# Kernel tuning notes

Hardware: AMD Instinct MI355X
Metric: run time of the kernel (lower is better)

## Reference

```python
import jax, jax.numpy as jnp
import numpy as np

MUL0, MUL1 = 32, 16          # multiplicities of 0e and 1o in irreps_node
RBF, HID = 16, 64
O1 = MUL0 * MUL0             # path 0e x 0e -> 0e
O2 = O1 + MUL0 * MUL1        # path 0e x 1o -> 1o
O3 = O2 + MUL1 * MUL1        # path 1o x 0e -> 1o
WNUMEL = O3 + MUL1 * MUL0    # path 1o x 1o -> 0e  => 2304 total
C_PATH = 1.0 / np.sqrt(MUL0 + MUL1).astype(np.float32)  # per-output fan-in norm
C_110 = 1.0 / np.sqrt(3.0)   # CG factor for 1o x 1o -> 0e (component norm)


def setup_inputs() -> dict:
    key = jax.random.key(0)
    ks = jax.random.split(key, 16)
    N, E = 50000, 200000
    x = jax.random.normal(ks[0], (N, MUL0 + 3 * MUL1), jnp.float32)
    edge_src = jax.random.randint(ks[1], (E,), 0, N)
    edge_dst = jax.random.randint(ks[2], (E,), 0, N)
    edge_sh = jax.random.normal(ks[3], (E, 4), jnp.float32)
    edge_rbf = jax.random.uniform(ks[4], (E, RBF), jnp.float32)
    # RadialMLP params (fan-in scaled init)
    w1 = jax.random.normal(ks[5], (RBF, HID), jnp.float32) / np.sqrt(RBF)
    b1 = jnp.zeros((HID,), jnp.float32)
    w2 = jax.random.normal(ks[6], (HID, HID), jnp.float32) / np.sqrt(HID)
    b2 = jnp.zeros((HID,), jnp.float32)
    w3 = jax.random.normal(ks[7], (HID, WNUMEL), jnp.float32) / np.sqrt(HID)
    b3 = jnp.zeros((WNUMEL,), jnp.float32)
    # o3.Linear weights (per-irrep mixing, fan-in normalization folded in)
    ws_self = jax.random.normal(ks[8], (MUL0, MUL0), jnp.float32) / np.sqrt(MUL0)
    wv_self = jax.random.normal(ks[9], (MUL1, MUL1), jnp.float32) / np.sqrt(MUL1)
    ws_out = jax.random.normal(ks[10], (MUL0, MUL0), jnp.float32) / np.sqrt(MUL0)
    wv_out = jax.random.normal(ks[11], (MUL1, MUL1), jnp.float32) / np.sqrt(MUL1)
    return {"x": x, "edge_src": edge_src, "edge_dst": edge_dst,
            "edge_sh": edge_sh, "edge_rbf": edge_rbf,
            "w1": w1, "b1": b1, "w2": w2, "b2": b2, "w3": w3, "b3": b3,
            "ws_self": ws_self, "wv_self": wv_self,
            "ws_out": ws_out, "wv_out": wv_out}


def _irrep_linear(x, ws, wv):
    # per-irrep mixing of '32x0e + 16x1o' features; x: [N, 80]
    n = x.shape[0]
    s = x[:, :MUL0] @ ws                                     # [N, 32]
    v = jnp.einsum('nid,io->nod', x[:, MUL0:].reshape(n, MUL1, 3), wv)
    return jnp.concatenate([s, v.reshape(n, 3 * MUL1)], axis=-1)


def reference(x, edge_src, edge_dst, edge_sh, edge_rbf,
              w1, b1, w2, b2, w3, b3, ws_self, wv_self, ws_out, wv_out):
    N = x.shape[0]
    E = edge_rbf.shape[0]
    # radial MLP -> per-edge TP weights [E, 2304]
    h = jax.nn.silu(edge_rbf @ w1 + b1)
    h = jax.nn.silu(h @ w2 + b2)
    W = h @ w3 + b3
    W1 = W[:, :O1].reshape(E, MUL0, MUL0)      # 0e x 0e -> 0e
    W2 = W[:, O1:O2].reshape(E, MUL0, MUL1)    # 0e x 1o -> 1o
    W3 = W[:, O2:O3].reshape(E, MUL1, MUL1)    # 1o x 0e -> 1o
    W4 = W[:, O3:].reshape(E, MUL1, MUL0)      # 1o x 1o -> 0e
    # gather source node features per edge
    xs = x[edge_src, :MUL0]                                   # [E, 32]
    xv = x[edge_src, MUL0:].reshape(E, MUL1, 3)               # [E, 16, 3]
    sh_s = edge_sh[:, 0]                                      # [E]
    sh_v = edge_sh[:, 1:4]                                    # [E, 3]
    # CG tensor product paths
    out_s = jnp.einsum('ei,eio->eo', xs * sh_s[:, None], W1)
    out_s = out_s + C_110 * jnp.einsum('eid,ed,eio->eo', xv, sh_v, W4)
    out_v = jnp.einsum('ei,ed,eio->eod', xs, sh_v, W2)
    out_v = out_v + jnp.einsum('eid,eio->eod', xv * sh_s[:, None, None], W3)
    m = C_PATH * jnp.concatenate([out_s, out_v.reshape(E, 3 * MUL1)], axis=-1)
    # scatter-add + degree normalize
    agg = jax.ops.segment_sum(m, edge_dst, num_segments=N)
    deg = jax.ops.segment_sum(jnp.ones((E,), x.dtype), edge_dst, num_segments=N)
    agg = agg / jnp.maximum(deg, 1.0)[:, None]
    return _irrep_linear(x, ws_self, wv_self) + _irrep_linear(agg, ws_out, wv_out)
```

## Files before the change

kernel.cpp:

```cpp
#include <hip/hip_runtime.h>
#include <math.h>

#define MUL0    32
#define MUL1    16
#define RBFD    16
#define HIDD    64
#define WNUMEL  2304
#define FDIM    80
#define CPATH   0.14433756729740643f
#define C110    0.57735026918962576f

#define TE       160
#define NTHREADS 320
#define NITER    48

#define W3N_ELEMS (NITER*6*512)
#define W1B_ELEMS (4*64*8)
#define W2B_ELEMS (4*2*64*8)

#define FS4_U16  0
#define XS_U16   2560
#define XV_U16   7680
#define SH_B     30720
#define SRC_B    33280
#define DST_B    33920
#define B3_B     34560
#define SMEM_B   43776

typedef float          f32x4   __attribute__((ext_vector_type(4)));
typedef short          short8  __attribute__((ext_vector_type(8)));
typedef short          short4v __attribute__((ext_vector_type(4)));
typedef unsigned short u16;

__device__ __forceinline__ float silu(float v) {
    return v / (1.0f + __expf(-v));
}
__device__ __forceinline__ u16 f2bf(float f) {
    unsigned int u = __float_as_uint(f);
    u += 0x7fffu + ((u >> 16) & 1u);
    return (u16)(u >> 16);
}
__device__ __forceinline__ float bf2f(u16 s) {
    return __uint_as_float(((unsigned int)s) << 16);
}
__device__ __forceinline__ f32x4 cvt4(short4v s) {
    f32x4 r;
    r[0] = bf2f((u16)s[0]); r[1] = bf2f((u16)s[1]);
    r[2] = bf2f((u16)s[2]); r[3] = bf2f((u16)s[3]);
    return r;
}
__device__ __forceinline__ f32x4 mfma16(short8 a, short8 b, f32x4 c) {
    return __builtin_amdgcn_mfma_f32_16x16x32_bf16(a, b, c, 0, 0, 0);
}

__device__ __forceinline__ int tile_of(int t, int pair) {
    if (t < 32) return (pair == 0) ? 2*t : (pair == 1) ? 2*t + 1 : 64 + t;
    int tt = t - 32;
    return (pair == 0) ? 112 + 2*tt : (pair == 1) ? 113 + 2*tt : 96 + tt;
}

__global__ void k_prep(const float* __restrict__ w3,
                       const float* __restrict__ w1,
                       const float* __restrict__ w2,
                       u16* __restrict__ w3n,
                       u16* __restrict__ w1b,
                       u16* __restrict__ w2b) {
    int idx = blockIdx.x * 256 + threadIdx.x;
    if (idx < W3N_ELEMS) {
        int j = idx & 7, l = (idx >> 3) & 63, f = idx >> 9;
        int t = f / 6, s = f - 6 * t, pair = s >> 1, kh = s & 1;
        int tile = tile_of(t, pair);
        int k = kh * 32 + 8 * (l >> 4) + j;
        int c = tile * 16 + (l & 15);
        w3n[idx] = f2bf(CPATH * w3[k * WNUMEL + c]);
        return;
    }
    idx -= W3N_ELEMS;
    if (idx < W1B_ELEMS) {
        int j = idx & 7, l = (idx >> 3) & 63, ct = idx >> 9;
        int k = 8 * (l >> 4) + j;
        int c = ct * 16 + (l & 15);
        w1b[idx] = (k < RBFD) ? f2bf(w1[k * HIDD + c]) : (u16)0;
        return;
    }
    idx -= W1B_ELEMS;
    if (idx < W2B_ELEMS) {
        int j = idx & 7, l = (idx >> 3) & 63, kh = (idx >> 9) & 1, ct = idx >> 10;
        int k = kh * 32 + 8 * (l >> 4) + j;
        int c = ct * 16 + (l & 15);
        w2b[idx] = f2bf(w2[k * HIDD + c]);
    }
}

#define COMPUTE(T, BP) do {                                                    \
    float bs0 = s_b3[(T)*48 + lo];                                             \
    float bs1 = s_b3[(T)*48 + 16 + lo];                                        \
    float bs2 = s_b3[(T)*48 + 32 + lo];                                        \
    _Pragma("unroll")                                                          \
    for (int rt = 0; rt < 2; ++rt) {                                           \
        const int fb = 2*w + rt;                                               \
        f32x4 tA = {bs0,bs0,bs0,bs0};                                          \
        tA = mfma16(a[rt][0], BP[0], tA); tA = mfma16(a[rt][1], BP[1], tA);    \
        f32x4 tB = {bs1,bs1,bs1,bs1};                                          \
        tB = mfma16(a[rt][0], BP[2], tB); tB = mfma16(a[rt][1], BP[3], tB);    \
        f32x4 tC = {bs2,bs2,bs2,bs2};                                          \
        tC = mfma16(a[rt][0], BP[4], tC); tC = mfma16(a[rt][1], BP[5], tC);    \
        if ((T) < 32) {                                                        \
            f32x4 fx = cvt4(*(const short4v*)&S[XS_U16 + fb*512 + (T)*16 + 4*g]); \
            f32x4 f1 = fx * sh0v[rt];                                          \
            acc[rt][0] += f1 * tA;                                             \
            acc[rt][1] += f1 * tB;                                             \
            acc[rt][2] += fx * tC;                                             \
        } else {                                                               \
            const int i_ = (T) - 32;                                           \
            f32x4 f4 = cvt4(*(const short4v*)&S[FS4_U16 + fb*256 + i_*16 + 4*g]); \
            acc[rt][0] += f4 * tA;                                             \
            acc[rt][1] += f4 * tB;                                             \
            acc[rt][3] += cvt4(*(const short4v*)&S[XV_U16 + fb*768 + (0 +i_)*16 + 4*g]) * tC; \
            acc[rt][4] += cvt4(*(const short4v*)&S[XV_U16 + fb*768 + (16+i_)*16 + 4*g]) * tC; \
            acc[rt][5] += cvt4(*(const short4v*)&S[XV_U16 + fb*768 + (32+i_)*16 + 4*g]) * tC; \
        }                                                                      \
    }                                                                          \
} while (0)

__global__ __launch_bounds__(NTHREADS)
void k_edge(const float* __restrict__ x,
            const int*   __restrict__ esrc,
            const int*   __restrict__ edst,
            const float* __restrict__ esh,
            const float* __restrict__ erbf,
            const u16*   __restrict__ w1b,
            const float* __restrict__ b1,
            const u16*   __restrict__ w2b,
            const float* __restrict__ b2,
            const u16*   __restrict__ w3n,
            const float* __restrict__ b3,
            float* __restrict__ agg,
            float* __restrict__ deg)
{
    __shared__ alignas(16) unsigned char smem[SMEM_B];
    u16*   S     = (u16*)smem;
    float* s_sh  = (float*)(smem + SH_B);
    int*   s_src = (int*)(smem + SRC_B);
    int*   s_dst = (int*)(smem + DST_B);
    float* s_b3  = (float*)(smem + B3_B);

    const int tid = threadIdx.x;
    const int eb  = blockIdx.x * TE;
    const int w   = tid >> 6;
    const int l   = tid & 63;
    const int lo  = l & 15;
    const int g   = l >> 4;

    if (tid < TE) {
        s_src[tid] = esrc[eb + tid];
        s_dst[tid] = edst[eb + tid];
    }
    for (int idx = tid; idx < TE * 4; idx += NTHREADS)
        s_sh[idx] = esh[eb * 4 + idx];
    __syncthreads();

    float cb1[4], cb2[4];
    #pragma unroll
    for (int ct = 0; ct < 4; ++ct) { cb1[ct] = b1[ct*16 + lo]; cb2[ct] = b2[ct*16 + lo]; }
    const short8* W1B = (const short8*)w1b;
    const short8* W2B = (const short8*)w2b;

    #pragma unroll
    for (int gr = 0; gr < 2; ++gr) {
        const int e0 = 32 * w + 16 * gr;
        short8 ar = {0,0,0,0,0,0,0,0};
        if (g < 2) {
            const float* rp = erbf + (size_t)(eb + e0 + lo) * RBFD + 8 * g;
            f32x4 r0 = *(const f32x4*)rp;
            f32x4 r1 = *(const f32x4*)(rp + 4);
            ar[0]=f2bf(r0[0]); ar[1]=f2bf(r0[1]); ar[2]=f2bf(r0[2]); ar[3]=f2bf(r0[3]);
            ar[4]=f2bf(r1[0]); ar[5]=f2bf(r1[1]); ar[6]=f2bf(r1[2]); ar[7]=f2bf(r1[3]);
        }
        #pragma unroll
        for (int ct = 0; ct < 4; ++ct) {
            f32x4 t = {cb1[ct], cb1[ct], cb1[ct], cb1[ct]};
            t = mfma16(ar, W1B[ct * 64 + l], t);
            #pragma unroll
            for (int r = 0; r < 4; ++r)
                S[(e0 + 4*g + r) * 72 + ct*16 + lo] = f2bf(silu(t[r]));
        }
    }
    #pragma unroll
    for (int gr = 0; gr < 2; ++gr) {
        const int e0 = 32 * w + 16 * gr;
        short8 a0 = *(const short8*)&S[(e0 + lo) * 72 + 0  + 8*g];
        short8 a1 = *(const short8*)&S[(e0 + lo) * 72 + 32 + 8*g];
        #pragma unroll
        for (int ct = 0; ct < 4; ++ct) {
            f32x4 t = {cb2[ct], cb2[ct], cb2[ct], cb2[ct]};
            t = mfma16(a0, W2B[(ct*2 + 0) * 64 + l], t);
            t = mfma16(a1, W2B[(ct*2 + 1) * 64 + l], t);
            #pragma unroll
            for (int r = 0; r < 4; ++r)
                S[(e0 + 4*g + r) * 72 + ct*16 + lo] = f2bf(silu(t[r]));
        }
    }
    short8 a[2][2];
    #pragma unroll
    for (int rt = 0; rt < 2; ++rt) {
        const int e0 = 32 * w + 16 * rt;
        a[rt][0] = *(const short8*)&S[(e0 + lo) * 72 + 0  + 8*g];
        a[rt][1] = *(const short8*)&S[(e0 + lo) * 72 + 32 + 8*g];
    }
    __syncthreads();

    if (tid < TE) {
        const int el = tid, grp = el >> 4, e16 = el & 15;
        const float sh0 = s_sh[el*4 + 0];
        const float sh1 = s_sh[el*4 + 1];
        const float sh2 = s_sh[el*4 + 2];
        const float sh3 = s_sh[el*4 + 3];
        const float* xrow = x + (size_t)s_src[el] * FDIM;
        u16* fs4B = S + FS4_U16 + grp * 256 + e16;
        u16* xsB  = S + XS_U16  + grp * 512 + e16;
        u16* xvB  = S + XV_U16  + grp * 768 + e16;
        #pragma unroll
        for (int v = 0; v < 8; ++v) {
            f32x4 x4 = *(const f32x4*)(xrow + 4 * v);
            #pragma unroll
            for (int c2 = 0; c2 < 4; ++c2)
                xsB[(4 * v + c2) * 16] = f2bf(x4[c2]);
        }
        float buf[48];
        #pragma unroll
        for (int v = 0; v < 12; ++v) {
            f32x4 t4 = *(const f32x4*)(xrow + MUL0 + 4 * v);
            buf[4*v]=t4[0]; buf[4*v+1]=t4[1]; buf[4*v+2]=t4[2]; buf[4*v+3]=t4[3];
        }
        #pragma unroll
        for (int i = 0; i < 16; ++i) {
            float v0 = buf[3*i], v1 = buf[3*i+1], v2 = buf[3*i+2];
            xvB[(0  + i) * 16] = f2bf(v0 * sh0);
            xvB[(16 + i) * 16] = f2bf(v1 * sh0);
            xvB[(32 + i) * 16] = f2bf(v2 * sh0);
            fs4B[i * 16]       = f2bf(C110 * (v0*sh1 + v1*sh2 + v2*sh3));
        }
    } else {
        for (int idx = tid - TE; idx < WNUMEL; idx += NTHREADS - TE) {
            int t = idx / 48, r = idx - 48 * t, pair = r >> 4, lo16 = r & 15;
            s_b3[idx] = CPATH * b3[tile_of(t, pair) * 16 + lo16];
        }
    }
    __syncthreads();

    f32x4 sh0v[2];
    #pragma unroll
    for (int rt = 0; rt < 2; ++rt)
        #pragma unroll
        for (int r = 0; r < 4; ++r)
            sh0v[rt][r] = s_sh[(32*w + 16*rt + 4*g + r) * 4];

    const short8* WB = (const short8*)w3n;
    f32x4 acc[2][6];
    #pragma unroll
    for (int rt = 0; rt < 2; ++rt)
        #pragma unroll
        for (int p = 0; p < 6; ++p) acc[rt][p] = (f32x4){0.f,0.f,0.f,0.f};

    short8 p0[6], p1[6];
    #pragma unroll
    for (int s = 0; s < 6; ++s) p0[s] = WB[s * 64 + l];

    for (int t = 0; t < NITER; t += 2) {
        #pragma unroll
        for (int s = 0; s < 6; ++s) p1[s] = WB[(t + 1) * 384 + s * 64 + l];
        COMPUTE(t, p0);
        {
            const int tn = (t + 2 < NITER) ? (t + 2) : 0;
            #pragma unroll
            for (int s = 0; s < 6; ++s) p0[s] = WB[tn * 384 + s * 64 + l];
        }
        COMPUTE(t + 1, p1);
    }

    #pragma unroll
    for (int rt = 0; rt < 2; ++rt) {
        #pragma unroll
        for (int r = 0; r < 4; ++r) {
            const int e_loc = 32*w + 16*rt + 4*g + r;
            float* row = agg + (size_t)s_dst[e_loc] * FDIM;
            float sv0 = s_sh[e_loc*4 + 1];
            float sv1 = s_sh[e_loc*4 + 2];
            float sv2 = s_sh[e_loc*4 + 3];
            atomicAdd(row + lo,      acc[rt][0][r]);
            atomicAdd(row + 16 + lo, acc[rt][1][r]);
            atomicAdd(row + MUL0 + lo*3 + 0, sv0*acc[rt][2][r] + acc[rt][3][r]);
            atomicAdd(row + MUL0 + lo*3 + 1, sv1*acc[rt][2][r] + acc[rt][4][r]);
            atomicAdd(row + MUL0 + lo*3 + 2, sv2*acc[rt][2][r] + acc[rt][5][r]);
        }
    }
    if (tid < TE) atomicAdd(deg + s_dst[tid], 1.0f);
}

#define NPB 16
__global__ __launch_bounds__(256)
void k_node(const float* __restrict__ x,
            const float* __restrict__ deg,
            const float* __restrict__ ws_self,
            const float* __restrict__ wv_self,
            const float* __restrict__ ws_out,
            const float* __restrict__ wv_out,
            float* __restrict__ out)
{
    __shared__ float s_x[NPB][81];
    __shared__ float s_a[NPB][81];
    __shared__ float s_inv[NPB];

    const int tid = threadIdx.x;
    const int n0  = blockIdx.x * NPB;

    if (tid < NPB) s_inv[tid] = 1.0f / fmaxf(deg[n0 + tid], 1.0f);
    const float* xb = x   + (size_t)n0 * FDIM;
    const float* ab = out + (size_t)n0 * FDIM;
    for (int idx = tid; idx < NPB * FDIM; idx += 256) {
        int nl = idx / FDIM, jj = idx - nl * FDIM;
        s_x[nl][jj] = xb[idx];
        s_a[nl][jj] = ab[idx];
    }
    __syncthreads();

    const int j  = tid & 15;
    const int nl = tid >> 4;
    const float inv = s_inv[nl];
    float* orow = out + (size_t)(n0 + nl) * FDIM;

    float s1s = 0.f, s1a = 0.f, s2s = 0.f, s2a = 0.f;
    #pragma unroll
    for (int i = 0; i < MUL0; ++i) {
        float xs = s_x[nl][i], as = s_a[nl][i];
        s1s += xs * ws_self[i * MUL0 + j];
        s1a += as * ws_out [i * MUL0 + j];
        s2s += xs * ws_self[i * MUL0 + j + 16];
        s2a += as * ws_out [i * MUL0 + j + 16];
    }
    orow[j]      = s1s + inv * s1a;
    orow[j + 16] = s2s + inv * s2a;

    float vs[3] = {0.f,0.f,0.f}, va[3] = {0.f,0.f,0.f};
    #pragma unroll
    for (int i = 0; i < MUL1; ++i) {
        float wsf = wv_self[i * MUL1 + j];
        float wof = wv_out [i * MUL1 + j];
        #pragma unroll
        for (int d = 0; d < 3; ++d) {
            vs[d] += s_x[nl][MUL0 + 3*i + d] * wsf;
            va[d] += s_a[nl][MUL0 + 3*i + d] * wof;
        }
    }
    #pragma unroll
    for (int d = 0; d < 3; ++d)
        orow[MUL0 + j*3 + d] = vs[d] + inv * va[d];
}

extern "C" void kernel_launch(void* const* d_in, const int* in_sizes, int n_in,
                              void* d_out, int out_size, void* d_ws, size_t ws_size,
                              hipStream_t stream)
{
    const float* x       = (const float*)d_in[0];
    const int*   esrc    = (const int*)  d_in[1];
    const int*   edst    = (const int*)  d_in[2];
    const float* esh     = (const float*)d_in[3];
    const float* erbf    = (const float*)d_in[4];
    const float* w1      = (const float*)d_in[5];
    const float* b1      = (const float*)d_in[6];
    const float* w2      = (const float*)d_in[7];
    const float* b2      = (const float*)d_in[8];
    const float* w3      = (const float*)d_in[9];
    const float* b3      = (const float*)d_in[10];
    const float* ws_self = (const float*)d_in[11];
    const float* wv_self = (const float*)d_in[12];
    const float* ws_out  = (const float*)d_in[13];
    const float* wv_out  = (const float*)d_in[14];

    const int N = in_sizes[0] / FDIM;
    const int E = in_sizes[1];

    char* wsp = (char*)d_ws;
    float* deg = (float*)wsp;
    size_t off = ((size_t)N * sizeof(float) + 255) & ~(size_t)255;
    u16* w3n = (u16*)(wsp + off);
    off += ((size_t)W3N_ELEMS * 2 + 255) & ~(size_t)255;
    u16* w1b = (u16*)(wsp + off);
    off += ((size_t)W1B_ELEMS * 2 + 255) & ~(size_t)255;
    u16* w2b = (u16*)(wsp + off);

    hipMemsetAsync(d_out, 0, (size_t)out_size * sizeof(float), stream);
    hipMemsetAsync(deg, 0, (size_t)N * sizeof(float), stream);

    k_prep<<<(W3N_ELEMS + W1B_ELEMS + W2B_ELEMS + 255) / 256, 256, 0, stream>>>(
        w3, w1, w2, w3n, w1b, w2b);

    k_edge<<<E / TE, NTHREADS, 0, stream>>>(
        x, esrc, edst, esh, erbf, w1b, b1, w2b, b2, w3n, b3,
        (float*)d_out, deg);

    k_node<<<N / NPB, 256, 0, stream>>>(
        x, deg, ws_self, wv_self, ws_out, wv_out, (float*)d_out);
}
```

Measured before the change: 269.3 us.

## Give each wave 64 edges to double W3 weight reuse per load

Each wavefront now processes four 16-edge row tiles instead of two, and the block shrinks to four waves handling 256 edges, with bounds checks for a partial final block. Each streamed W3 weight fragment is therefore reused across twice as many edges, halving global weight traffic per edge. A periodic s_barrier inside the main loop keeps the waves in step so their weight loads hit cache together. The cost is more accumulator registers (RT*6 f32x4), larger LDS use (about 63 KB), and fewer waves, which may reduce occupancy and latency hiding.

```diff
diff --git a/kernel.cpp b/kernel.cpp
--- a/kernel.cpp
+++ b/kernel.cpp
@@ -10,8 +10,9 @@
 #define CPATH   0.14433756729740643f
 #define C110    0.57735026918962576f
 
-#define TE       160
-#define NTHREADS 320
+#define TE       256
+#define NTHREADS 256
+#define RT       4
 #define NITER    48
 
 #define W3N_ELEMS (NITER*6*512)
@@ -19,13 +20,13 @@
 #define W2B_ELEMS (4*2*64*8)
 
 #define FS4_U16  0
-#define XS_U16   2560
-#define XV_U16   7680
-#define SH_B     30720
-#define SRC_B    33280
-#define DST_B    33920
-#define B3_B     34560
-#define SMEM_B   43776
+#define XS_U16   4096
+#define XV_U16   12288
+#define SH_B     49152
+#define SRC_B    53248
+#define DST_B    54272
+#define B3_B     55296
+#define SMEM_B   64512
 
 typedef float          f32x4   __attribute__((ext_vector_type(4)));
 typedef short          short8  __attribute__((ext_vector_type(8)));
@@ -97,8 +98,8 @@
     float bs1 = s_b3[(T)*48 + 16 + lo];                                        \
     float bs2 = s_b3[(T)*48 + 32 + lo];                                        \
     _Pragma("unroll")                                                          \
-    for (int rt = 0; rt < 2; ++rt) {                                           \
-        const int fb = 2*w + rt;                                               \
+    for (int rt = 0; rt < RT; ++rt) {                                          \
+        const int fb = RT*w + rt;                                              \
         f32x4 tA = {bs0,bs0,bs0,bs0};                                          \
         tA = mfma16(a[rt][0], BP[0], tA); tA = mfma16(a[rt][1], BP[1], tA);    \
         f32x4 tB = {bs1,bs1,bs1,bs1};                                          \
@@ -136,7 +137,8 @@
             const u16*   __restrict__ w3n,
             const float* __restrict__ b3,
             float* __restrict__ agg,
-            float* __restrict__ deg)
+            float* __restrict__ deg,
+            int E)
 {
     __shared__ alignas(16) unsigned char smem[SMEM_B];
     u16*   S     = (u16*)smem;
@@ -152,12 +154,15 @@
     const int lo  = l & 15;
     const int g   = l >> 4;
 
-    if (tid < TE) {
-        s_src[tid] = esrc[eb + tid];
-        s_dst[tid] = edst[eb + tid];
-    }
-    for (int idx = tid; idx < TE * 4; idx += NTHREADS)
-        s_sh[idx] = esh[eb * 4 + idx];
+    {
+        int eg = eb + tid;
+        s_src[tid] = (eg < E) ? esrc[eg] : 0;
+        s_dst[tid] = (eg < E) ? edst[eg] : 0;
+    }
+    for (int idx = tid; idx < TE * 4; idx += NTHREADS) {
+        long eg4 = (long)eb * 4 + idx;
+        s_sh[idx] = (eg4 < (long)E * 4) ? esh[eg4] : 0.0f;
+    }
     __syncthreads();
 
     float cb1[4], cb2[4];
@@ -167,10 +172,10 @@
     const short8* W2B = (const short8*)w2b;
 
     #pragma unroll
-    for (int gr = 0; gr < 2; ++gr) {
-        const int e0 = 32 * w + 16 * gr;
+    for (int gr = 0; gr < RT; ++gr) {
+        const int e0 = 64 * w + 16 * gr;
         short8 ar = {0,0,0,0,0,0,0,0};
-        if (g < 2) {
+        if (g < 2 && (eb + e0 + lo) < E) {
             const float* rp = erbf + (size_t)(eb + e0 + lo) * RBFD + 8 * g;
             f32x4 r0 = *(const f32x4*)rp;
             f32x4 r1 = *(const f32x4*)(rp + 4);
@@ -187,8 +192,8 @@
         }
     }
     #pragma unroll
-    for (int gr = 0; gr < 2; ++gr) {
-        const int e0 = 32 * w + 16 * gr;
+    for (int gr = 0; gr < RT; ++gr) {
+        const int e0 = 64 * w + 16 * gr;
         short8 a0 = *(const short8*)&S[(e0 + lo) * 72 + 0  + 8*g];
         short8 a1 = *(const short8*)&S[(e0 + lo) * 72 + 32 + 8*g];
         #pragma unroll
@@ -201,16 +206,16 @@
                 S[(e0 + 4*g + r) * 72 + ct*16 + lo] = f2bf(silu(t[r]));
         }
     }
-    short8 a[2][2];
-    #pragma unroll
-    for (int rt = 0; rt < 2; ++rt) {
-        const int e0 = 32 * w + 16 * rt;
+    short8 a[RT][2];
+    #pragma unroll
+    for (int rt = 0; rt < RT; ++rt) {
+        const int e0 = 64 * w + 16 * rt;
         a[rt][0] = *(const short8*)&S[(e0 + lo) * 72 + 0  + 8*g];
         a[rt][1] = *(const short8*)&S[(e0 + lo) * 72 + 32 + 8*g];
     }
     __syncthreads();
 
-    if (tid < TE) {
+    {
         const int el = tid, grp = el >> 4, e16 = el & 15;
         const float sh0 = s_sh[el*4 + 0];
         const float sh1 = s_sh[el*4 + 1];
@@ -241,25 +246,24 @@
             xvB[(32 + i) * 16] = f2bf(v2 * sh0);
             fs4B[i * 16]       = f2bf(C110 * (v0*sh1 + v1*sh2 + v2*sh3));
         }
-    } else {
-        for (int idx = tid - TE; idx < WNUMEL; idx += NTHREADS - TE) {
-            int t = idx / 48, r = idx - 48 * t, pair = r >> 4, lo16 = r & 15;
-            s_b3[idx] = CPATH * b3[tile_of(t, pair) * 16 + lo16];
-        }
+    }
+    for (int idx = tid; idx < WNUMEL; idx += NTHREADS) {
+        int t = idx / 48, r = idx - 48 * t, pair = r >> 4, lo16 = r & 15;
+        s_b3[idx] = CPATH * b3[tile_of(t, pair) * 16 + lo16];
     }
     __syncthreads();
 
-    f32x4 sh0v[2];
-    #pragma unroll
-    for (int rt = 0; rt < 2; ++rt)
+    f32x4 sh0v[RT];
+    #pragma unroll
+    for (int rt = 0; rt < RT; ++rt)
         #pragma unroll
         for (int r = 0; r < 4; ++r)
-            sh0v[rt][r] = s_sh[(32*w + 16*rt + 4*g + r) * 4];
+            sh0v[rt][r] = s_sh[(64*w + 16*rt + 4*g + r) * 4];
 
     const short8* WB = (const short8*)w3n;
-    f32x4 acc[2][6];
-    #pragma unroll
-    for (int rt = 0; rt < 2; ++rt)
+    f32x4 acc[RT][6];
+    #pragma unroll
+    for (int rt = 0; rt < RT; ++rt)
         #pragma unroll
         for (int p = 0; p < 6; ++p) acc[rt][p] = (f32x4){0.f,0.f,0.f,0.f};
 
@@ -268,6 +272,7 @@
     for (int s = 0; s < 6; ++s) p0[s] = WB[s * 64 + l];
 
     for (int t = 0; t < NITER; t += 2) {
+        if (t && (t & 3) == 0) __builtin_amdgcn_s_barrier();
         #pragma unroll
         for (int s = 0; s < 6; ++s) p1[s] = WB[(t + 1) * 384 + s * 64 + l];
         COMPUTE(t, p0);
@@ -280,10 +285,10 @@
     }
 
     #pragma unroll
-    for (int rt = 0; rt < 2; ++rt) {
+    for (int rt = 0; rt < RT; ++rt) {
         #pragma unroll
         for (int r = 0; r < 4; ++r) {
-            const int e_loc = 32*w + 16*rt + 4*g + r;
+            const int e_loc = 64*w + 16*rt + 4*g + r;
             float* row = agg + (size_t)s_dst[e_loc] * FDIM;
             float sv0 = s_sh[e_loc*4 + 1];
             float sv1 = s_sh[e_loc*4 + 2];
@@ -295,7 +300,7 @@
             atomicAdd(row + MUL0 + lo*3 + 2, sv2*acc[rt][2][r] + acc[rt][5][r]);
         }
     }
-    if (tid < TE) atomicAdd(deg + s_dst[tid], 1.0f);
+    if ((eb + tid) < E) atomicAdd(deg + s_dst[tid], 1.0f);
 }
 
 #define NPB 16
@@ -396,9 +401,10 @@
     k_prep<<<(W3N_ELEMS + W1B_ELEMS + W2B_ELEMS + 255) / 256, 256, 0, stream>>>(
         w3, w1, w2, w3n, w1b, w2b);
 
-    k_edge<<<E / TE, NTHREADS, 0, stream>>>(
+    const int nblk = (E + TE - 1) / TE;
+    k_edge<<<nblk, NTHREADS, 0, stream>>>(
         x, esrc, edst, esh, erbf, w1b, b1, w2b, b2, w3n, b3,
-        (float*)d_out, deg);
+        (float*)d_out, deg, E);
 
     k_node<<<N / NPB, 256, 0, stream>>>(
         x, deg, ws_self, wv_self, ws_out, wv_out, (float*)d_out);
```

Result: slower. 357.9 us (+32.9%).

## Stage gathered edge features in fp32 LDS and hoist sh0 scaling out of loop

Applied to the files above, without the earlier changes.

Gathered node features (xs, xv*sh0, and the 1o·1o contraction term) are now kept in LDS as fp32 instead of bf16. This removes per-iteration bf16-to-fp32 conversions in the inner loop and the bf16 rounding of those operands. The sh0 multiply for the first 32 tiles is moved out of the loop and applied once to the accumulators at t==32. A periodic s_barrier every 4 iterations is added to keep waves in step for weight-cache locality. The cost is that LDS per block grows from about 43KB to about 74KB, which may lower occupancy.

```diff
diff --git a/kernel.cpp b/kernel.cpp
--- a/kernel.cpp
+++ b/kernel.cpp
@@ -18,18 +18,17 @@
 #define W1B_ELEMS (4*64*8)
 #define W2B_ELEMS (4*2*64*8)
 
-#define FS4_U16  0
-#define XS_U16   2560
-#define XV_U16   7680
-#define SH_B     30720
-#define SRC_B    33280
-#define DST_B    33920
-#define B3_B     34560
-#define SMEM_B   43776
+#define XS_F     0
+#define XV_F     5120
+#define FS4_F    12800
+#define SH_B     61440
+#define SRC_B    64000
+#define DST_B    64640
+#define B3_B     65280
+#define SMEM_B   74496
 
 typedef float          f32x4   __attribute__((ext_vector_type(4)));
 typedef short          short8  __attribute__((ext_vector_type(8)));
-typedef short          short4v __attribute__((ext_vector_type(4)));
 typedef unsigned short u16;
 
 __device__ __forceinline__ float silu(float v) {
@@ -39,15 +38,6 @@
     unsigned int u = __float_as_uint(f);
     u += 0x7fffu + ((u >> 16) & 1u);
     return (u16)(u >> 16);
-}
-__device__ __forceinline__ float bf2f(u16 s) {
-    return __uint_as_float(((unsigned int)s) << 16);
-}
-__device__ __forceinline__ f32x4 cvt4(short4v s) {
-    f32x4 r;
-    r[0] = bf2f((u16)s[0]); r[1] = bf2f((u16)s[1]);
-    r[2] = bf2f((u16)s[2]); r[3] = bf2f((u16)s[3]);
-    return r;
 }
 __device__ __forceinline__ f32x4 mfma16(short8 a, short8 b, f32x4 c) {
     return __builtin_amdgcn_mfma_f32_16x16x32_bf16(a, b, c, 0, 0, 0);
@@ -106,19 +96,18 @@
         f32x4 tC = {bs2,bs2,bs2,bs2};                                          \
         tC = mfma16(a[rt][0], BP[4], tC); tC = mfma16(a[rt][1], BP[5], tC);    \
         if ((T) < 32) {                                                        \
-            f32x4 fx = cvt4(*(const short4v*)&S[XS_U16 + fb*512 + (T)*16 + 4*g]); \
-            f32x4 f1 = fx * sh0v[rt];                                          \
-            acc[rt][0] += f1 * tA;                                             \
-            acc[rt][1] += f1 * tB;                                             \
+            f32x4 fx = *(const f32x4*)&Sf[XS_F + fb*512 + (T)*16 + 4*g];       \
+            acc[rt][0] += fx * tA;                                             \
+            acc[rt][1] += fx * tB;                                             \
             acc[rt][2] += fx * tC;                                             \
         } else {                                                               \
             const int i_ = (T) - 32;                                           \
-            f32x4 f4 = cvt4(*(const short4v*)&S[FS4_U16 + fb*256 + i_*16 + 4*g]); \
+            f32x4 f4 = *(const f32x4*)&Sf[FS4_F + fb*256 + i_*16 + 4*g];       \
             acc[rt][0] += f4 * tA;                                             \
             acc[rt][1] += f4 * tB;                                             \
-            acc[rt][3] += cvt4(*(const short4v*)&S[XV_U16 + fb*768 + (0 +i_)*16 + 4*g]) * tC; \
-            acc[rt][4] += cvt4(*(const short4v*)&S[XV_U16 + fb*768 + (16+i_)*16 + 4*g]) * tC; \
-            acc[rt][5] += cvt4(*(const short4v*)&S[XV_U16 + fb*768 + (32+i_)*16 + 4*g]) * tC; \
+            acc[rt][3] += (*(const f32x4*)&Sf[XV_F + fb*768 + (0 +i_)*16 + 4*g]) * tC; \
+            acc[rt][4] += (*(const f32x4*)&Sf[XV_F + fb*768 + (16+i_)*16 + 4*g]) * tC; \
+            acc[rt][5] += (*(const f32x4*)&Sf[XV_F + fb*768 + (32+i_)*16 + 4*g]) * tC; \
         }                                                                      \
     }                                                                          \
 } while (0)
@@ -140,6 +129,7 @@
 {
     __shared__ alignas(16) unsigned char smem[SMEM_B];
     u16*   S     = (u16*)smem;
+    float* Sf    = (float*)smem;
     float* s_sh  = (float*)(smem + SH_B);
     int*   s_src = (int*)(smem + SRC_B);
     int*   s_dst = (int*)(smem + DST_B);
@@ -217,15 +207,15 @@
         const float sh2 = s_sh[el*4 + 2];
         const float sh3 = s_sh[el*4 + 3];
         const float* xrow = x + (size_t)s_src[el] * FDIM;
-        u16* fs4B = S + FS4_U16 + grp * 256 + e16;
-        u16* xsB  = S + XS_U16  + grp * 512 + e16;
-        u16* xvB  = S + XV_U16  + grp * 768 + e16;
+        float* xsB  = Sf + XS_F  + grp * 512 + e16;
+        float* xvB  = Sf + XV_F  + grp * 768 + e16;
+        float* fs4B = Sf + FS4_F + grp * 256 + e16;
         #pragma unroll
         for (int v = 0; v < 8; ++v) {
             f32x4 x4 = *(const f32x4*)(xrow + 4 * v);
             #pragma unroll
             for (int c2 = 0; c2 < 4; ++c2)
-                xsB[(4 * v + c2) * 16] = f2bf(x4[c2]);
+                xsB[(4 * v + c2) * 16] = x4[c2];
         }
         float buf[48];
         #pragma unroll
@@ -236,10 +226,10 @@
         #pragma unroll
         for (int i = 0; i < 16; ++i) {
             float v0 = buf[3*i], v1 = buf[3*i+1], v2 = buf[3*i+2];
-            xvB[(0  + i) * 16] = f2bf(v0 * sh0);
-            xvB[(16 + i) * 16] = f2bf(v1 * sh0);
-            xvB[(32 + i) * 16] = f2bf(v2 * sh0);
-            fs4B[i * 16]       = f2bf(C110 * (v0*sh1 + v1*sh2 + v2*sh3));
+            xvB[(0  + i) * 16] = v0 * sh0;
+            xvB[(16 + i) * 16] = v1 * sh0;
+            xvB[(32 + i) * 16] = v2 * sh0;
+            fs4B[i * 16]       = C110 * (v0*sh1 + v1*sh2 + v2*sh3);
         }
     } else {
         for (int idx = tid - TE; idx < WNUMEL; idx += NTHREADS - TE) {
@@ -268,6 +258,14 @@
     for (int s = 0; s < 6; ++s) p0[s] = WB[s * 64 + l];
 
     for (int t = 0; t < NITER; t += 2) {
+        if (t == 32) {
+            #pragma unroll
+            for (int rt = 0; rt < 2; ++rt) {
+                acc[rt][0] *= sh0v[rt];
+                acc[rt][1] *= sh0v[rt];
+            }
+        }
+        if (t && (t & 3) == 0) __builtin_amdgcn_s_barrier();
         #pragma unroll
         for (int s = 0; s < 6; ++s) p1[s] = WB[(t + 1) * 384 + s * 64 + l];
         COMPUTE(t, p0);
```

Result: slower. 281.7 us (+4.6%).
